# Kernel tuning notes

Hardware: AMD Instinct MI355X
Metric: run time of the kernel (lower is better)

The kernel has to match this reference:

```python
import jax, jax.numpy as jnp
import numpy as np

EPS = 1e-7
K = 15      # kernel_size
CIN = 128
F = 256


def setup_inputs() -> dict:
    key = jax.random.key(0)
    k1, k2 = jax.random.split(key)
    x = jax.random.normal(k1, (32, 4096, CIN), dtype=jnp.float32)
    # glorot-uniform init then UnitNorm over axes (0,1) per filter, matching the constraint
    limit = np.sqrt(6.0 / (K * CIN + F))
    kernel = jax.random.uniform(k2, (K, CIN, F), dtype=jnp.float32, minval=-limit, maxval=limit)
    kernel = kernel / jnp.sqrt(jnp.sum(kernel * kernel, axis=(0, 1), keepdims=True) + 1e-12)
    scale = jnp.full((1, 1, 1), 10.0, dtype=jnp.float32)
    bias = jnp.zeros((F,), dtype=jnp.float32)
    return {"inputs": x, "kernel": kernel, "scale": scale, "bias": bias}


def reference(inputs, kernel, scale, bias):
    # dot-product conv: (B, L-K+1, F), VALID padding, stride 1
    dot = jax.lax.conv_general_dilated(
        inputs, kernel, window_strides=(1,), padding="VALID",
        dimension_numbers=("NWC", "WIO", "NWC"))
    # sliding sum-of-squares over window*channels. In the original this is a
    # conv1d with an all-ones (K,CIN,F) kernel, i.e. every filter sees the same
    # scalar sum -> compute it once via a cumsum box filter and broadcast.
    k = kernel.shape[0]
    sq = jnp.sum(inputs * inputs, axis=-1)                       # (B, L)
    cs = jnp.cumsum(jnp.pad(sq, ((0, 0), (1, 0))), axis=1)       # (B, L+1)
    win = cs[:, k:] - cs[:, :-k]                                 # (B, L-K+1)
    norm_x = jnp.sqrt(win + EPS)[..., None]                      # (B, L-K+1, 1)
    return scale * (dot / norm_x) + bias
```

## Files before the change

kernel.cpp:

```cpp
#include <hip/hip_runtime.h>
#include <hip/hip_bf16.h>
#include <stdint.h>

#define K_TAPS 15
#define CIN    128
#define F_OUT  256
#define LSEQ   4096
#define LOUT   (LSEQ - K_TAPS + 1)
#define BATCH  32

typedef __attribute__((ext_vector_type(8))) short bf16x8;
typedef __attribute__((ext_vector_type(4))) float f32x4;

typedef __attribute__((address_space(1))) const unsigned int gu32_t;
typedef __attribute__((address_space(3))) unsigned int su32_t;

__global__ void prep_w_kernel(const float* __restrict__ W,
                              unsigned short* __restrict__ Wp) {
  int idx = blockIdx.x * 256 + threadIdx.x;
  int f  = idx & 255;
  int kc = idx >> 8;
  int c  = kc & 127;
  int k  = kc >> 7;
  float w = W[idx];
  __hip_bfloat16 hb = __float2bfloat16(w);
  int chalf = c >> 6;
  int c6    = c & 63;
  int slot  = ((c6 >> 3) ^ f) & 7;
  int cp    = slot * 8 + (c & 7);
  Wp[((size_t)(k * 2 + chalf) * 256 + f) * 64 + cp] =
      *reinterpret_cast<unsigned short*>(&hb);
}

__global__ void sq_kernel(const float* __restrict__ x, float* __restrict__ sq) {
  int wid  = threadIdx.x >> 6;
  int lane = threadIdx.x & 63;
  int half = lane >> 5;
  int lq   = lane & 31;
  long pos = (long)blockIdx.x * 8 + wid * 2 + half;
  const float4* xp = (const float4*)(x + pos * CIN) + lq;
  float4 v = *xp;
  float s = v.x * v.x + v.y * v.y + v.z * v.z + v.w * v.w;
  #pragma unroll
  for (int m = 1; m <= 16; m <<= 1) s += __shfl_xor(s, m, 64);
  if (lq == 0) sq[pos] = s;
}

__global__ void rn_kernel(const float* __restrict__ sq,
                          const float* __restrict__ scale,
                          float* __restrict__ rn) {
  int t = blockIdx.x * 256 + threadIdx.x;
  int b = blockIdx.y;
  if (t >= LOUT) return;
  const float* s = sq + b * LSEQ + t;
  float w = 0.f;
  #pragma unroll
  for (int k = 0; k < K_TAPS; ++k) w += s[k];
  rn[b * LSEQ + t] = scale[0] / sqrtf(w + 1e-7f);
}

#define BM 128
#define BN 128
#define XROWS 144
#define XBYTES (XROWS * 256)
#define BBYTES 16384
#define NPHASE (K_TAPS * 2)

__global__ __launch_bounds__(256, 2) void conv_gemm_kernel(
    const float* __restrict__ x, const unsigned short* __restrict__ Wp,
    const float* __restrict__ rn, const float* __restrict__ bias,
    float* __restrict__ out)
{
  __shared__ __align__(16) char lds[XBYTES + 2 * BBYTES];
  char* Xs = lds;
  char* Bs = lds + XBYTES;

  const int b     = blockIdx.y;
  const int mtile = blockIdx.x >> 1;
  const int ntile = blockIdx.x & 1;
  const int t0    = mtile * BM;
  const int n0    = ntile * BN;

  const int tx   = threadIdx.x;
  const int wid  = tx >> 6;
  const int lane = tx & 63;
  const int wm   = wid >> 1;
  const int wn   = wid & 1;

  auto stageB = [&](int buf, int phase) {
    const char* src = (const char*)Wp + (size_t)phase * 32768
                      + (size_t)n0 * 128;
    char* dst = Bs + buf * BBYTES;
    int base = wid * 4096;
    #pragma unroll
    for (int i = 0; i < 4; ++i) {
      int off = base + i * 1024;
      __builtin_amdgcn_global_load_lds(
          (gu32_t*)(src + off + lane * 16),
          (su32_t*)(dst + off), 16, 0, 0);
    }
  };

  stageB(0, 0);

  {
    const int rloc = tx >> 4;
    const int g    = tx & 15;
    const float* xb = x + (long)b * LSEQ * CIN;
    #pragma unroll
    for (int it = 0; it < 9; ++it) {
      int row  = it * 16 + rloc;
      int grow = t0 + row;
      float v[8];
      if (grow < LSEQ) {
        const float4* p = (const float4*)(xb + (long)grow * CIN + g * 8);
        float4 a0 = p[0], a1 = p[1];
        v[0]=a0.x; v[1]=a0.y; v[2]=a0.z; v[3]=a0.w;
        v[4]=a1.x; v[5]=a1.y; v[6]=a1.z; v[7]=a1.w;
      } else {
        #pragma unroll
        for (int j = 0; j < 8; ++j) v[j] = 0.f;
      }
      union { unsigned short us[8]; int4 q; } pk;
      #pragma unroll
      for (int j = 0; j < 8; ++j) {
        __hip_bfloat16 hb = __float2bfloat16(v[j]);
        pk.us[j] = *reinterpret_cast<unsigned short*>(&hb);
      }
      int slot = (g & 8) | ((g ^ row) & 7);
      *(int4*)(Xs + row * 256 + slot * 16) = pk.q;
    }
  }
  __syncthreads();

  f32x4 acc[4][4] = {};

  const int klane = lane >> 4;
  const int rl    = lane & 15;
  const int arow0 = wm * 64;
  const int bcol0 = wn * 64;

  #pragma unroll 2
  for (int ph = 0; ph < NPHASE; ++ph) {
    const int buf = ph & 1;
    const int tap = ph >> 1;
    const int kk0 = (ph & 1) * 2;

    if (ph + 1 < NPHASE) stageB(buf ^ 1, ph + 1);

    bf16x8 af[2][4];
    #pragma unroll
    for (int j = 0; j < 2; ++j) {
      const int ga = (kk0 + j) * 4 + klane;
      #pragma unroll
      for (int mf = 0; mf < 4; ++mf) {
        int row  = arow0 + mf * 16 + rl + tap;
        int slot = (ga & 8) | ((ga ^ row) & 7);
        af[j][mf] = *(const bf16x8*)(Xs + row * 256 + slot * 16);
      }
    }

    if (ph + 1 < NPHASE) {
      asm volatile("s_waitcnt vmcnt(4)" ::: "memory");
    } else {
      asm volatile("s_waitcnt vmcnt(0)" ::: "memory");
    }
    __builtin_amdgcn_s_barrier();

    const char* Bsc = Bs + buf * BBYTES;
    bf16x8 bfr[2][4];
    #pragma unroll
    for (int j = 0; j < 2; ++j) {
      const int gb = ((kk0 + j) & 1) * 4 + klane;
      #pragma unroll
      for (int nf = 0; nf < 4; ++nf) {
        int fc   = bcol0 + nf * 16 + rl;
        int slot = (gb ^ fc) & 7;
        bfr[j][nf] = *(const bf16x8*)(Bsc + fc * 128 + slot * 16);
      }
    }

    __builtin_amdgcn_s_setprio(1);
    #pragma unroll
    for (int j = 0; j < 2; ++j)
      #pragma unroll
      for (int mf = 0; mf < 4; ++mf)
        #pragma unroll
        for (int nf = 0; nf < 4; ++nf)
          acc[mf][nf] = __builtin_amdgcn_mfma_f32_16x16x32_bf16(
              af[j][mf], bfr[j][nf], acc[mf][nf], 0, 0, 0);
    __builtin_amdgcn_s_setprio(0);

    asm volatile("s_waitcnt lgkmcnt(0)" ::: "memory");
    __builtin_amdgcn_s_barrier();
  }

  const int rgrp = lane >> 4;
  float biasv[4];
  #pragma unroll
  for (int nf = 0; nf < 4; ++nf) biasv[nf] = bias[n0 + bcol0 + nf * 16 + rl];
  float* ob = out + (long)b * LOUT * F_OUT;
  const float* rnb = rn + b * LSEQ + t0;
  #pragma unroll
  for (int mf = 0; mf < 4; ++mf) {
    #pragma unroll
    for (int r = 0; r < 4; ++r) {
      int row = arow0 + mf * 16 + rgrp * 4 + r;
      int gt  = t0 + row;
      if (gt < LOUT) {
        float rv = rnb[row];
        #pragma unroll
        for (int nf = 0; nf < 4; ++nf) {
          ob[(long)gt * F_OUT + n0 + bcol0 + nf * 16 + rl] =
              acc[mf][nf][r] * rv + biasv[nf];
        }
      }
    }
  }
}

extern "C" void kernel_launch(void* const* d_in, const int* in_sizes, int n_in,
                              void* d_out, int out_size, void* d_ws, size_t ws_size,
                              hipStream_t stream) {
  const float* x     = (const float*)d_in[0];
  const float* W     = (const float*)d_in[1];
  const float* scale = (const float*)d_in[2];
  const float* bias  = (const float*)d_in[3];
  float* out = (float*)d_out;

  char* ws = (char*)d_ws;
  unsigned short* Wp = (unsigned short*)ws;
  float* sq = (float*)(ws + 1048576);
  float* rn = (float*)(ws + 1048576 + 524288);

  prep_w_kernel<<<1920, 256, 0, stream>>>(W, Wp);
  sq_kernel<<<BATCH * LSEQ / 8, 256, 0, stream>>>(x, sq);
  rn_kernel<<<dim3((LOUT + 255) / 256, BATCH), 256, 0, stream>>>(sq, scale, rn);
  conv_gemm_kernel<<<dim3(64, BATCH), 256, 0, stream>>>(x, Wp, rn, bias, out);
}
```

Baseline: 147.5 us.

## Fuse sum-of-squares norm into conv GEMM and change weight/LDS layouts

Removes the separate sq and rn kernels. The conv GEMM now accumulates per-row squared sums while it stages x into LDS, then computes the 15-tap window norm in shared memory. This drops two launches and the full extra read of x (16 MB). The packed weight layout also changes to group-major with an unswizzled B tile in LDS, the X swizzle becomes a full 4-bit XOR, and the rn window is recomputed redundantly for each n-tile (two per row tile). The unswizzled B reads could add LDS bank conflicts.

```diff
diff --git a/kernel.cpp b/kernel.cpp
--- a/kernel.cpp
+++ b/kernel.cpp
@@ -24,39 +24,11 @@
   int k  = kc >> 7;
   float w = W[idx];
   __hip_bfloat16 hb = __float2bfloat16(w);
-  int chalf = c >> 6;
-  int c6    = c & 63;
-  int slot  = ((c6 >> 3) ^ f) & 7;
-  int cp    = slot * 8 + (c & 7);
-  Wp[((size_t)(k * 2 + chalf) * 256 + f) * 64 + cp] =
+  int ht = k * 2 + (c >> 6);
+  int g  = (c >> 3) & 7;
+  int c7 = c & 7;
+  Wp[(((size_t)ht * 8 + g) * 256 + f) * 8 + c7] =
       *reinterpret_cast<unsigned short*>(&hb);
-}
-
-__global__ void sq_kernel(const float* __restrict__ x, float* __restrict__ sq) {
-  int wid  = threadIdx.x >> 6;
-  int lane = threadIdx.x & 63;
-  int half = lane >> 5;
-  int lq   = lane & 31;
-  long pos = (long)blockIdx.x * 8 + wid * 2 + half;
-  const float4* xp = (const float4*)(x + pos * CIN) + lq;
-  float4 v = *xp;
-  float s = v.x * v.x + v.y * v.y + v.z * v.z + v.w * v.w;
-  #pragma unroll
-  for (int m = 1; m <= 16; m <<= 1) s += __shfl_xor(s, m, 64);
-  if (lq == 0) sq[pos] = s;
-}
-
-__global__ void rn_kernel(const float* __restrict__ sq,
-                          const float* __restrict__ scale,
-                          float* __restrict__ rn) {
-  int t = blockIdx.x * 256 + threadIdx.x;
-  int b = blockIdx.y;
-  if (t >= LOUT) return;
-  const float* s = sq + b * LSEQ + t;
-  float w = 0.f;
-  #pragma unroll
-  for (int k = 0; k < K_TAPS; ++k) w += s[k];
-  rn[b * LSEQ + t] = scale[0] / sqrtf(w + 1e-7f);
 }
 
 #define BM 128
@@ -68,10 +40,12 @@
 
 __global__ __launch_bounds__(256, 2) void conv_gemm_kernel(
     const float* __restrict__ x, const unsigned short* __restrict__ Wp,
-    const float* __restrict__ rn, const float* __restrict__ bias,
+    const float* __restrict__ scale, const float* __restrict__ bias,
     float* __restrict__ out)
 {
   __shared__ __align__(16) char lds[XBYTES + 2 * BBYTES];
+  __shared__ float sqs[XROWS];
+  __shared__ float rns[BM];
   char* Xs = lds;
   char* Bs = lds + XBYTES;
 
@@ -87,17 +61,19 @@
   const int wm   = wid >> 1;
   const int wn   = wid & 1;
 
+  const float scalev = scale[0];
+
   auto stageB = [&](int buf, int phase) {
-    const char* src = (const char*)Wp + (size_t)phase * 32768
-                      + (size_t)n0 * 128;
+    const char* src = (const char*)Wp + (size_t)phase * 32768;
     char* dst = Bs + buf * BBYTES;
-    int base = wid * 4096;
     #pragma unroll
     for (int i = 0; i < 4; ++i) {
-      int off = base + i * 1024;
+      int slot = i * 256 + tx;
+      int g    = slot >> 7;
+      int floc = slot & 127;
       __builtin_amdgcn_global_load_lds(
-          (gu32_t*)(src + off + lane * 16),
-          (su32_t*)(dst + off), 16, 0, 0);
+          (gu32_t*)(src + ((size_t)g * 256 + n0 + floc) * 16),
+          (su32_t*)(dst + (size_t)slot * 16), 16, 0, 0);
     }
   };
 
@@ -121,17 +97,31 @@
         #pragma unroll
         for (int j = 0; j < 8; ++j) v[j] = 0.f;
       }
+      float s = 0.f;
       union { unsigned short us[8]; int4 q; } pk;
       #pragma unroll
       for (int j = 0; j < 8; ++j) {
+        s += v[j] * v[j];
         __hip_bfloat16 hb = __float2bfloat16(v[j]);
         pk.us[j] = *reinterpret_cast<unsigned short*>(&hb);
       }
-      int slot = (g & 8) | ((g ^ row) & 7);
+      int slot = (g ^ row) & 15;
       *(int4*)(Xs + row * 256 + slot * 16) = pk.q;
+      s += __shfl_xor(s, 1, 16);
+      s += __shfl_xor(s, 2, 16);
+      s += __shfl_xor(s, 4, 16);
+      s += __shfl_xor(s, 8, 16);
+      if (g == 0) sqs[row] = s;
     }
   }
   __syncthreads();
+
+  if (tx < BM) {
+    float wsum = 0.f;
+    #pragma unroll
+    for (int k = 0; k < K_TAPS; ++k) wsum += sqs[tx + k];
+    rns[tx] = scalev / sqrtf(wsum + 1e-7f);
+  }
 
   f32x4 acc[4][4] = {};
 
@@ -155,7 +145,7 @@
       #pragma unroll
       for (int mf = 0; mf < 4; ++mf) {
         int row  = arow0 + mf * 16 + rl + tap;
-        int slot = (ga & 8) | ((ga ^ row) & 7);
+        int slot = (ga ^ row) & 15;
         af[j][mf] = *(const bf16x8*)(Xs + row * 256 + slot * 16);
       }
     }
@@ -174,9 +164,8 @@
       const int gb = ((kk0 + j) & 1) * 4 + klane;
       #pragma unroll
       for (int nf = 0; nf < 4; ++nf) {
-        int fc   = bcol0 + nf * 16 + rl;
-        int slot = (gb ^ fc) & 7;
-        bfr[j][nf] = *(const bf16x8*)(Bsc + fc * 128 + slot * 16);
+        int floc = bcol0 + nf * 16 + rl;
+        bfr[j][nf] = *(const bf16x8*)(Bsc + ((size_t)gb * 128 + floc) * 16);
       }
     }
 
@@ -200,7 +189,6 @@
   #pragma unroll
   for (int nf = 0; nf < 4; ++nf) biasv[nf] = bias[n0 + bcol0 + nf * 16 + rl];
   float* ob = out + (long)b * LOUT * F_OUT;
-  const float* rnb = rn + b * LSEQ + t0;
   #pragma unroll
   for (int mf = 0; mf < 4; ++mf) {
     #pragma unroll
@@ -208,7 +196,7 @@
       int row = arow0 + mf * 16 + rgrp * 4 + r;
       int gt  = t0 + row;
       if (gt < LOUT) {
-        float rv = rnb[row];
+        float rv = rns[row];
         #pragma unroll
         for (int nf = 0; nf < 4; ++nf) {
           ob[(long)gt * F_OUT + n0 + bcol0 + nf * 16 + rl] =
@@ -228,13 +216,8 @@
   const float* bias  = (const float*)d_in[3];
   float* out = (float*)d_out;
 
-  char* ws = (char*)d_ws;
-  unsigned short* Wp = (unsigned short*)ws;
-  float* sq = (float*)(ws + 1048576);
-  float* rn = (float*)(ws + 1048576 + 524288);
+  unsigned short* Wp = (unsigned short*)d_ws;
 
   prep_w_kernel<<<1920, 256, 0, stream>>>(W, Wp);
-  sq_kernel<<<BATCH * LSEQ / 8, 256, 0, stream>>>(x, sq);
-  rn_kernel<<<dim3((LOUT + 255) / 256, BATCH), 256, 0, stream>>>(sq, scale, rn);
-  conv_gemm_kernel<<<dim3(64, BATCH), 256, 0, stream>>>(x, Wp, rn, bias, out);
+  conv_gemm_kernel<<<dim3(64, BATCH), 256, 0, stream>>>(x, Wp, scale, bias, out);
 }
```

After: 158.9 us. 1.08x slower.

## Enlarge conv GEMM tile to 256x256 with 512-thread blocks and split MFMA phases

Applied to the files above, without the earlier changes.

The block tile grows from 128x128 to 256 output rows by all 256 filters, with 8 waves each computing a 128x64 sub-tile. Each 64-channel step is broken into four barrier-separated sub-phases of LDS loads and MFMAs. The goal is more input and weight reuse per LDS byte, less halo reloading and fewer blocks. The cost is a much larger LDS footprint, about 132 KB per block, which likely allows only one block per CU. It also doubles the accumulator registers and adds more barriers per step.

```diff
diff --git a/kernel.cpp b/kernel.cpp
--- a/kernel.cpp
+++ b/kernel.cpp
@@ -59,14 +59,14 @@
   rn[b * LSEQ + t] = scale[0] / sqrtf(w + 1e-7f);
 }
 
-#define BM 128
-#define BN 128
-#define XROWS 144
+#define BM 256
+#define BN 256
+#define XROWS 272
 #define XBYTES (XROWS * 256)
-#define BBYTES 16384
-#define NPHASE (K_TAPS * 2)
-
-__global__ __launch_bounds__(256, 2) void conv_gemm_kernel(
+#define BBYTES 32768
+#define NSTEP (K_TAPS * 2)
+
+__global__ __launch_bounds__(512, 2) void conv_gemm_kernel(
     const float* __restrict__ x, const unsigned short* __restrict__ Wp,
     const float* __restrict__ rn, const float* __restrict__ bias,
     float* __restrict__ out)
@@ -75,26 +75,26 @@
   char* Xs = lds;
   char* Bs = lds + XBYTES;
 
-  const int b     = blockIdx.y;
-  const int mtile = blockIdx.x >> 1;
-  const int ntile = blockIdx.x & 1;
-  const int t0    = mtile * BM;
-  const int n0    = ntile * BN;
+  const int b  = blockIdx.y;
+  const int t0 = blockIdx.x * BM;
 
   const int tx   = threadIdx.x;
   const int wid  = tx >> 6;
   const int lane = tx & 63;
-  const int wm   = wid >> 1;
-  const int wn   = wid & 1;
-
-  auto stageB = [&](int buf, int phase) {
-    const char* src = (const char*)Wp + (size_t)phase * 32768
-                      + (size_t)n0 * 128;
+  const int wm   = wid >> 2;
+  const int wn   = wid & 3;
+
+  const int klane = lane >> 4;
+  const int rl    = lane & 15;
+  const int arow0 = wm * 128;
+  const int bcol0 = wn * 64;
+
+  auto stageB = [&](int buf, int step) {
+    const char* src = (const char*)Wp + (size_t)step * 32768;
     char* dst = Bs + buf * BBYTES;
-    int base = wid * 4096;
     #pragma unroll
     for (int i = 0; i < 4; ++i) {
-      int off = base + i * 1024;
+      int off = i * 8192 + wid * 1024;
       __builtin_amdgcn_global_load_lds(
           (gu32_t*)(src + off + lane * 16),
           (su32_t*)(dst + off), 16, 0, 0);
@@ -109,100 +109,150 @@
     const float* xb = x + (long)b * LSEQ * CIN;
     #pragma unroll
     for (int it = 0; it < 9; ++it) {
-      int row  = it * 16 + rloc;
+      int row  = it * 32 + rloc;
       int grow = t0 + row;
-      float v[8];
-      if (grow < LSEQ) {
-        const float4* p = (const float4*)(xb + (long)grow * CIN + g * 8);
-        float4 a0 = p[0], a1 = p[1];
-        v[0]=a0.x; v[1]=a0.y; v[2]=a0.z; v[3]=a0.w;
-        v[4]=a1.x; v[5]=a1.y; v[6]=a1.z; v[7]=a1.w;
-      } else {
+      if (row < XROWS) {
+        float v[8];
+        if (grow < LSEQ) {
+          const float4* p = (const float4*)(xb + (long)grow * CIN + g * 8);
+          float4 a0 = p[0], a1 = p[1];
+          v[0]=a0.x; v[1]=a0.y; v[2]=a0.z; v[3]=a0.w;
+          v[4]=a1.x; v[5]=a1.y; v[6]=a1.z; v[7]=a1.w;
+        } else {
+          #pragma unroll
+          for (int j = 0; j < 8; ++j) v[j] = 0.f;
+        }
+        union { unsigned short us[8]; int4 q; } pk;
         #pragma unroll
-        for (int j = 0; j < 8; ++j) v[j] = 0.f;
-      }
-      union { unsigned short us[8]; int4 q; } pk;
-      #pragma unroll
-      for (int j = 0; j < 8; ++j) {
-        __hip_bfloat16 hb = __float2bfloat16(v[j]);
-        pk.us[j] = *reinterpret_cast<unsigned short*>(&hb);
-      }
-      int slot = (g & 8) | ((g ^ row) & 7);
-      *(int4*)(Xs + row * 256 + slot * 16) = pk.q;
+        for (int j = 0; j < 8; ++j) {
+          __hip_bfloat16 hb = __float2bfloat16(v[j]);
+          pk.us[j] = *reinterpret_cast<unsigned short*>(&hb);
+        }
+        int slot = (g & 8) | ((g ^ row) & 7);
+        *(int4*)(Xs + row * 256 + slot * 16) = pk.q;
+      }
     }
   }
   __syncthreads();
 
-  f32x4 acc[4][4] = {};
-
-  const int klane = lane >> 4;
-  const int rl    = lane & 15;
-  const int arow0 = wm * 64;
-  const int bcol0 = wn * 64;
+  f32x4 acc[8][4] = {};
 
   #pragma unroll 2
-  for (int ph = 0; ph < NPHASE; ++ph) {
-    const int buf = ph & 1;
-    const int tap = ph >> 1;
-    const int kk0 = (ph & 1) * 2;
-
-    if (ph + 1 < NPHASE) stageB(buf ^ 1, ph + 1);
-
-    bf16x8 af[2][4];
-    #pragma unroll
-    for (int j = 0; j < 2; ++j) {
-      const int ga = (kk0 + j) * 4 + klane;
-      #pragma unroll
-      for (int mf = 0; mf < 4; ++mf) {
-        int row  = arow0 + mf * 16 + rl + tap;
-        int slot = (ga & 8) | ((ga ^ row) & 7);
-        af[j][mf] = *(const bf16x8*)(Xs + row * 256 + slot * 16);
-      }
-    }
-
-    if (ph + 1 < NPHASE) {
-      asm volatile("s_waitcnt vmcnt(4)" ::: "memory");
-    } else {
-      asm volatile("s_waitcnt vmcnt(0)" ::: "memory");
-    }
-    __builtin_amdgcn_s_barrier();
-
-    const char* Bsc = Bs + buf * BBYTES;
-    bf16x8 bfr[2][4];
-    #pragma unroll
-    for (int j = 0; j < 2; ++j) {
-      const int gb = ((kk0 + j) & 1) * 4 + klane;
+  for (int s = 0; s < NSTEP; ++s) {
+    const int tap = s >> 1;
+    const int ch8 = (s & 1) * 8;
+    const char* Bsc = Bs + (s & 1) * BBYTES;
+
+    bf16x8 afA[4], afB[4], bfr0[4], bfr1[4];
+
+    {
+      const int ga = ch8 + klane;
+      #pragma unroll
+      for (int i = 0; i < 4; ++i) {
+        int row  = arow0 + i * 16 + rl + tap;
+        int slot = (ga & 8) | ((ga ^ row) & 7);
+        afA[i] = *(const bf16x8*)(Xs + row * 256 + slot * 16);
+      }
+      #pragma unroll
+      for (int nf = 0; nf < 4; ++nf) {
+        int fc   = bcol0 + nf * 16 + rl;
+        int slot = (klane ^ fc) & 7;
+        bfr0[nf] = *(const bf16x8*)(Bsc + fc * 128 + slot * 16);
+      }
+      if (s + 1 < NSTEP) stageB((s & 1) ^ 1, s + 1);
+    }
+    __builtin_amdgcn_s_barrier();
+    asm volatile("s_waitcnt lgkmcnt(0)" ::: "memory");
+    __builtin_amdgcn_s_setprio(1);
+    #pragma unroll
+    for (int i = 0; i < 4; ++i)
+      #pragma unroll
+      for (int nf = 0; nf < 4; ++nf)
+        acc[i][nf] = __builtin_amdgcn_mfma_f32_16x16x32_bf16(
+            afA[i], bfr0[nf], acc[i][nf], 0, 0, 0);
+    __builtin_amdgcn_s_setprio(0);
+    __builtin_amdgcn_s_barrier();
+
+    {
+      const int ga = ch8 + klane;
+      #pragma unroll
+      for (int i = 0; i < 4; ++i) {
+        int row  = arow0 + (i + 4) * 16 + rl + tap;
+        int slot = (ga & 8) | ((ga ^ row) & 7);
+        afB[i] = *(const bf16x8*)(Xs + row * 256 + slot * 16);
+      }
+    }
+    __builtin_amdgcn_s_barrier();
+    asm volatile("s_waitcnt lgkmcnt(0)" ::: "memory");
+    __builtin_amdgcn_s_setprio(1);
+    #pragma unroll
+    for (int i = 0; i < 4; ++i)
+      #pragma unroll
+      for (int nf = 0; nf < 4; ++nf)
+        acc[i + 4][nf] = __builtin_amdgcn_mfma_f32_16x16x32_bf16(
+            afB[i], bfr0[nf], acc[i + 4][nf], 0, 0, 0);
+    __builtin_amdgcn_s_setprio(0);
+    __builtin_amdgcn_s_barrier();
+
+    {
+      const int ga = ch8 + 4 + klane;
+      const int gb = 4 + klane;
+      #pragma unroll
+      for (int i = 0; i < 4; ++i) {
+        int row  = arow0 + i * 16 + rl + tap;
+        int slot = (ga & 8) | ((ga ^ row) & 7);
+        afA[i] = *(const bf16x8*)(Xs + row * 256 + slot * 16);
+      }
       #pragma unroll
       for (int nf = 0; nf < 4; ++nf) {
         int fc   = bcol0 + nf * 16 + rl;
         int slot = (gb ^ fc) & 7;
-        bfr[j][nf] = *(const bf16x8*)(Bsc + fc * 128 + slot * 16);
-      }
-    }
-
-    __builtin_amdgcn_s_setprio(1);
-    #pragma unroll
-    for (int j = 0; j < 2; ++j)
-      #pragma unroll
-      for (int mf = 0; mf < 4; ++mf)
-        #pragma unroll
-        for (int nf = 0; nf < 4; ++nf)
-          acc[mf][nf] = __builtin_amdgcn_mfma_f32_16x16x32_bf16(
-              af[j][mf], bfr[j][nf], acc[mf][nf], 0, 0, 0);
-    __builtin_amdgcn_s_setprio(0);
-
-    asm volatile("s_waitcnt lgkmcnt(0)" ::: "memory");
+        bfr1[nf] = *(const bf16x8*)(Bsc + fc * 128 + slot * 16);
+      }
+    }
+    __builtin_amdgcn_s_barrier();
+    asm volatile("s_waitcnt lgkmcnt(0)" ::: "memory");
+    __builtin_amdgcn_s_setprio(1);
+    #pragma unroll
+    for (int i = 0; i < 4; ++i)
+      #pragma unroll
+      for (int nf = 0; nf < 4; ++nf)
+        acc[i][nf] = __builtin_amdgcn_mfma_f32_16x16x32_bf16(
+            afA[i], bfr1[nf], acc[i][nf], 0, 0, 0);
+    __builtin_amdgcn_s_setprio(0);
+    __builtin_amdgcn_s_barrier();
+
+    {
+      const int ga = ch8 + 4 + klane;
+      #pragma unroll
+      for (int i = 0; i < 4; ++i) {
+        int row  = arow0 + (i + 4) * 16 + rl + tap;
+        int slot = (ga & 8) | ((ga ^ row) & 7);
+        afB[i] = *(const bf16x8*)(Xs + row * 256 + slot * 16);
+      }
+    }
+    __builtin_amdgcn_s_barrier();
+    asm volatile("s_waitcnt lgkmcnt(0)" ::: "memory");
+    __builtin_amdgcn_s_setprio(1);
+    #pragma unroll
+    for (int i = 0; i < 4; ++i)
+      #pragma unroll
+      for (int nf = 0; nf < 4; ++nf)
+        acc[i + 4][nf] = __builtin_amdgcn_mfma_f32_16x16x32_bf16(
+            afB[i], bfr0 == bfr1 ? bfr1[nf] : bfr1[nf], acc[i + 4][nf], 0, 0, 0);
+    __builtin_amdgcn_s_setprio(0);
+    asm volatile("s_waitcnt vmcnt(0)" ::: "memory");
     __builtin_amdgcn_s_barrier();
   }
 
   const int rgrp = lane >> 4;
   float biasv[4];
   #pragma unroll
-  for (int nf = 0; nf < 4; ++nf) biasv[nf] = bias[n0 + bcol0 + nf * 16 + rl];
+  for (int nf = 0; nf < 4; ++nf) biasv[nf] = bias[bcol0 + nf * 16 + rl];
   float* ob = out + (long)b * LOUT * F_OUT;
   const float* rnb = rn + b * LSEQ + t0;
   #pragma unroll
-  for (int mf = 0; mf < 4; ++mf) {
+  for (int mf = 0; mf < 8; ++mf) {
     #pragma unroll
     for (int r = 0; r < 4; ++r) {
       int row = arow0 + mf * 16 + rgrp * 4 + r;
@@ -211,7 +261,7 @@
         float rv = rnb[row];
         #pragma unroll
         for (int nf = 0; nf < 4; ++nf) {
-          ob[(long)gt * F_OUT + n0 + bcol0 + nf * 16 + rl] =
+          ob[(long)gt * F_OUT + bcol0 + nf * 16 + rl] =
               acc[mf][nf][r] * rv + biasv[nf];
         }
       }
@@ -236,5 +286,5 @@
   prep_w_kernel<<<1920, 256, 0, stream>>>(W, Wp);
   sq_kernel<<<BATCH * LSEQ / 8, 256, 0, stream>>>(x, sq);
   rn_kernel<<<dim3((LOUT + 255) / 256, BATCH), 256, 0, stream>>>(sq, scale, rn);
-  conv_gemm_kernel<<<dim3(64, BATCH), 256, 0, stream>>>(x, Wp, rn, bias, out);
-}
+  conv_gemm_kernel<<<dim3(16, BATCH), 512, 0, stream>>>(x, Wp, rn, bias, out);
+}
```

Measured after the change: 148.1 us. Within noise of the previous version (+0.4%).
